# Kernel optimization log

Hardware: AMD Instinct MI355X
Metric: run time of the kernel (lower is better)

The kernel has to match this reference:

```python
import jax, jax.numpy as jnp
import numpy as np

NENTITY, NRELATION, EMB_DIM, K = 200000, 500, 512, 2
BATCH = 8192


@jax.custom_vjp
def sign_ste(x):
    return jnp.sign(x)

def _sign_fwd(x):
    return jnp.sign(x), None

def _sign_bwd(_, g):
    return (g,)  # straight-through estimator: identity gradient

sign_ste.defvjp(_sign_fwd, _sign_bwd)


def setup_inputs() -> dict:
    key = jax.random.key(0)
    k1, k2, k3, k4, k5, k6 = jax.random.split(key, 6)
    return {
        "head_idx": jax.random.randint(k1, (BATCH,), 0, NENTITY),
        "relation_idx": jax.random.randint(k2, (BATCH,), 0, NRELATION),
        "tail_idx": jax.random.randint(k3, (BATCH,), 0, NENTITY),
        # parameters, init per nn.init.uniform_(a=-1, b=1)
        "entity_embedding": jax.random.uniform(k4, (NENTITY, EMB_DIM, 1, K), jnp.float32, -1.0, 1.0),
        "relation_embedding": jax.random.uniform(k5, (NRELATION, EMB_DIM, K), jnp.float32, -1.0, 1.0),
        "alpha_embedding": jax.random.uniform(k6, (NRELATION, EMB_DIM), jnp.float32, -1.0, 1.0),
    }


def reference(head_idx, relation_idx, tail_idx, entity_embedding, relation_embedding, alpha_embedding):
    # gathers
    heads = entity_embedding[head_idx, :, 0, :]      # [B, D, 2]
    tails = entity_embedding[tail_idx, :, 0, :]      # [B, D, 2]
    relations = relation_embedding[relation_idx]     # [B, D, 2]
    alphas = alpha_embedding[relation_idx]           # [B, D]

    x = sign_ste(relations[:, :, 0])                 # [B, D]
    y = sign_ste(relations[:, :, 1])
    a = sign_ste(alphas)

    s = (x + y) * 0.5
    d = (x - y) * 0.5
    # 2x2 matrix: [[s, -d*a], [d, s*a]] applied as h^T M t, done elementwise
    h0, h1 = heads[:, :, 0], heads[:, :, 1]
    t0, t1 = tails[:, :, 0], tails[:, :, 1]
    # score_bd = h0*(M00*t0 + M01*t1) + h1*(M10*t0 + M11*t1)
    score = h0 * (s * t0 - d * a * t1) + h1 * (d * t0 + s * a * t1)  # [B, D]
    return jnp.sqrt(jnp.sum(score * score, axis=1))                   # [B]
```

## Files before the change

kernel.cpp:

```cpp
#include <hip/hip_runtime.h>


__device__ __forceinline__ float sgn(float x) {
    return (x > 0.f) ? 1.f : ((x < 0.f) ? -1.f : 0.f);
}

__global__ __launch_bounds__(256) void DKSTE_85315230367936_kernel(
    const int* __restrict__ head_idx,
    const int* __restrict__ rel_idx,
    const int* __restrict__ tail_idx,
    const float* __restrict__ ent,
    const float* __restrict__ rel,
    const float* __restrict__ alpha,
    float* __restrict__ out,
    int batch)
{
    const int wave = threadIdx.x >> 6;
    const int lane = threadIdx.x & 63;
    const int b = blockIdx.x * 4 + wave;
    if (b >= batch) return;

    const long long h = head_idx[b];
    const long long t = tail_idx[b];
    const long long r = rel_idx[b];

    const float4* __restrict__ hrow = (const float4*)(ent + h * 1024ll);
    const float4* __restrict__ trow = (const float4*)(ent + t * 1024ll);
    const float4* __restrict__ rrow = (const float4*)(rel + r * 1024ll);
    const float2* __restrict__ arow = (const float2*)(alpha + r * 512ll);

    float acc = 0.f;
#pragma unroll
    for (int j = 0; j < 4; ++j) {
        const int i = lane + 64 * j;
        const float4 hv = hrow[i];
        const float4 tv = trow[i];
        const float4 rv = rrow[i];
        const float2 av = arow[i];

        {
            const float sx = sgn(rv.x), sy = sgn(rv.y), sa = sgn(av.x);
            const float s = (sx + sy) * 0.5f;
            const float d = (sx - sy) * 0.5f;
            const float sc = hv.x * (s * tv.x - d * sa * tv.y)
                           + hv.y * (d * tv.x + s * sa * tv.y);
            acc = fmaf(sc, sc, acc);
        }
        {
            const float sx = sgn(rv.z), sy = sgn(rv.w), sa = sgn(av.y);
            const float s = (sx + sy) * 0.5f;
            const float d = (sx - sy) * 0.5f;
            const float sc = hv.z * (s * tv.z - d * sa * tv.w)
                           + hv.w * (d * tv.z + s * sa * tv.w);
            acc = fmaf(sc, sc, acc);
        }
    }

#pragma unroll
    for (int off = 32; off; off >>= 1)
        acc += __shfl_xor(acc, off, 64);

    if (lane == 0)
        out[b] = sqrtf(acc);
}

extern "C" void kernel_launch(void* const* d_in, const int* in_sizes, int n_in,
                              void* d_out, int out_size, void* d_ws, size_t ws_size,
                              hipStream_t stream) {
    const int*   head_idx = (const int*)d_in[0];
    const int*   rel_idx  = (const int*)d_in[1];
    const int*   tail_idx = (const int*)d_in[2];
    const float* ent      = (const float*)d_in[3];
    const float* rel      = (const float*)d_in[4];
    const float* alpha    = (const float*)d_in[5];
    float*       out      = (float*)d_out;

    const int batch = in_sizes[0];
    const int blocks = (batch + 3) / 4;

    DKSTE_85315230367936_kernel<<<blocks, 256, 0, stream>>>(
        head_idx, rel_idx, tail_idx, ent, rel, alpha, out, batch);
}
```

Baseline: 19.82 us.

## Pre-pack relation and alpha signs into bytes via a separate kernel

Adds a pre-pass kernel that turns the relation and alpha tables into 2-bit sign codes, one byte per dimension, stored in the workspace. The main kernel then reads 2 bytes per lane per iteration instead of 24 bytes of float relation and alpha data, and makes the batch index wave-uniform with readfirstlane. The cost is an extra launch that reads all 500x512x3 floats every call, plus a dependency between the two kernels. Because relation rows are heavily reused across the batch and were probably already cache-resident, the saving may be smaller than the added pass.

```diff
diff --git a/kernel.cpp b/kernel.cpp
--- a/kernel.cpp
+++ b/kernel.cpp
@@ -1,8 +1,27 @@
 #include <hip/hip_runtime.h>
 
 
-__device__ __forceinline__ float sgn(float x) {
-    return (x > 0.f) ? 1.f : ((x < 0.f) ? -1.f : 0.f);
+__global__ __launch_bounds__(256) void pack_rel_kernel(
+    const float* __restrict__ rel,
+    const float* __restrict__ alpha,
+    unsigned char* __restrict__ packed,
+    int nrel)
+{
+    const int r = blockIdx.x;
+    if (r >= nrel) return;
+    for (int d = threadIdx.x; d < 512; d += 256) {
+        const float x = rel[(size_t)r * 1024 + d * 2];
+        const float y = rel[(size_t)r * 1024 + d * 2 + 1];
+        const float a = alpha[(size_t)r * 512 + d];
+        const unsigned sx = (x > 0.f) ? 2u : ((x < 0.f) ? 0u : 1u);
+        const unsigned sy = (y > 0.f) ? 2u : ((y < 0.f) ? 0u : 1u);
+        const unsigned sa = (a > 0.f) ? 2u : ((a < 0.f) ? 0u : 1u);
+        packed[(size_t)r * 512 + d] = (unsigned char)(sx | (sy << 2) | (sa << 4));
+    }
+}
+
+__device__ __forceinline__ float dec2(unsigned v) {
+    return (float)((int)(v & 3u) - 1);
 }
 
 __global__ __launch_bounds__(256) void DKSTE_85315230367936_kernel(
@@ -10,15 +29,15 @@
     const int* __restrict__ rel_idx,
     const int* __restrict__ tail_idx,
     const float* __restrict__ ent,
-    const float* __restrict__ rel,
-    const float* __restrict__ alpha,
+    const unsigned char* __restrict__ packed,
     float* __restrict__ out,
     int batch)
 {
     const int wave = threadIdx.x >> 6;
     const int lane = threadIdx.x & 63;
-    const int b = blockIdx.x * 4 + wave;
+    int b = blockIdx.x * 4 + wave;
     if (b >= batch) return;
+    b = __builtin_amdgcn_readfirstlane(b);
 
     const long long h = head_idx[b];
     const long long t = tail_idx[b];
@@ -26,8 +45,8 @@
 
     const float4* __restrict__ hrow = (const float4*)(ent + h * 1024ll);
     const float4* __restrict__ trow = (const float4*)(ent + t * 1024ll);
-    const float4* __restrict__ rrow = (const float4*)(rel + r * 1024ll);
-    const float2* __restrict__ arow = (const float2*)(alpha + r * 512ll);
+    const unsigned short* __restrict__ prow =
+        (const unsigned short*)(packed + r * 512ll);
 
     float acc = 0.f;
 #pragma unroll
@@ -35,11 +54,11 @@
         const int i = lane + 64 * j;
         const float4 hv = hrow[i];
         const float4 tv = trow[i];
-        const float4 rv = rrow[i];
-        const float2 av = arow[i];
+        const unsigned pk = prow[i];
 
         {
-            const float sx = sgn(rv.x), sy = sgn(rv.y), sa = sgn(av.x);
+            const unsigned c = pk & 0xffu;
+            const float sx = dec2(c), sy = dec2(c >> 2), sa = dec2(c >> 4);
             const float s = (sx + sy) * 0.5f;
             const float d = (sx - sy) * 0.5f;
             const float sc = hv.x * (s * tv.x - d * sa * tv.y)
@@ -47,7 +66,8 @@
             acc = fmaf(sc, sc, acc);
         }
         {
-            const float sx = sgn(rv.z), sy = sgn(rv.w), sa = sgn(av.y);
+            const unsigned c = pk >> 8;
+            const float sx = dec2(c), sy = dec2(c >> 2), sa = dec2(c >> 4);
             const float s = (sx + sy) * 0.5f;
             const float d = (sx - sy) * 0.5f;
             const float sc = hv.z * (s * tv.z - d * sa * tv.w)
@@ -74,10 +94,14 @@
     const float* rel      = (const float*)d_in[4];
     const float* alpha    = (const float*)d_in[5];
     float*       out      = (float*)d_out;
+    unsigned char* packed = (unsigned char*)d_ws;
 
     const int batch = in_sizes[0];
+    const int nrel  = in_sizes[4] / 1024;
+
+    pack_rel_kernel<<<nrel, 256, 0, stream>>>(rel, alpha, packed, nrel);
+
     const int blocks = (batch + 3) / 4;
-
     DKSTE_85315230367936_kernel<<<blocks, 256, 0, stream>>>(
-        head_idx, rel_idx, tail_idx, ent, rel, alpha, out, batch);
+        head_idx, rel_idx, tail_idx, ent, packed, out, batch);
 }
```

Measured after the change: 22.18 us. 1.12x slower.
